# Kernel tuning notes

Measured on AMD Instinct MI355X. Metric: run time of the kernel, lower is better.

The kernel has to match this reference:

```python
import jax, jax.numpy as jnp
import numpy as np

K = 16          # NUM_PARTS (foreground parts); K+1 prototypes incl. background
D = 768         # EMBED_DIM
C = 200         # NUM_CLASSES
LN_EPS = 1e-6


def setup_inputs() -> dict:
    key = jax.random.key(0)
    k1, k2, k3, k4 = jax.random.split(key, 4)
    B, H, W = 32, 24, 24
    patch_features = jax.random.normal(k1, (B, H, W, D), dtype=jnp.float32)
    prototypes = 0.02 * jax.random.normal(k2, (K + 1, D), dtype=jnp.float32)
    ln_gamma = jnp.ones((D,), dtype=jnp.float32)
    ln_beta = jnp.zeros((D,), dtype=jnp.float32)
    # keras Dense default: glorot_uniform kernel, zero bias
    lim = np.sqrt(6.0 / (D + C)).astype(np.float32)
    w_cls = jax.random.uniform(k3, (D, C), dtype=jnp.float32, minval=-lim, maxval=lim)
    b_cls = jnp.zeros((C,), dtype=jnp.float32)
    return {
        "patch_features": patch_features,
        "prototypes": prototypes,
        "ln_gamma": ln_gamma,
        "ln_beta": ln_beta,
        "w_cls": w_cls,
        "b_cls": b_cls,
    }


def reference(patch_features, prototypes, ln_gamma, ln_beta, w_cls, b_cls):
    B, H, W, Dm = patch_features.shape
    P = H * W
    x = patch_features.reshape(B, P, Dm)                      # (B,P,D)

    # squared euclidean distance to K+1 prototypes, expressed as a GEMM:
    # ||z - p||^2 = ||z||^2 - 2 z.p + ||p||^2   -> (B,P,K+1)
    x_sq = jnp.sum(x * x, axis=-1, keepdims=True)             # (B,P,1)
    p_sq = jnp.sum(prototypes * prototypes, axis=-1)          # (K+1,)
    xp = jnp.einsum("bpd,kd->bpk", x, prototypes)             # (B,P,K+1)
    dists = x_sq - 2.0 * xp + p_sq                            # (B,P,K+1)

    # eval path: plain softmax over -distances
    a = jax.nn.softmax(-dists, axis=-1)                       # (B,P,K+1)

    # attention maps (B, K+1, H, W)
    A = jnp.transpose(a, (0, 2, 1)).reshape(B, K + 1, H, W)

    # weighted aggregation of patch features per part, normalized by P
    v_all = jnp.einsum("bpk,bpd->bkd", a, x) / jnp.float32(P) # (B,K+1,D)
    v_fg = v_all[:, :K, :]                                    # (B,K,D)

    # layernorm over last axis (eps=1e-6, learnable gamma/beta)
    mu = jnp.mean(v_fg, axis=-1, keepdims=True)
    var = jnp.mean(jnp.square(v_fg - mu), axis=-1, keepdims=True)
    v_norm = (v_fg - mu) * jax.lax.rsqrt(var + LN_EPS) * ln_gamma + ln_beta

    # shared per-part classifier + mean aggregation over parts
    logits_parts = jnp.einsum("bkd,dc->bkc", v_norm, w_cls) + b_cls  # (B,K,C)
    logits_agg = jnp.mean(logits_parts, axis=1)                      # (B,C)

    return (A, v_norm, logits_parts, logits_agg)
```

## Files before the change

### kernel.cpp

```cpp
#include <hip/hip_runtime.h>
#include <hip/hip_bf16.h>

#define B    32
#define P    576
#define D    768
#define K1   17
#define KFG  16
#define C    200
#define LN_EPS 1e-6f

typedef __attribute__((ext_vector_type(8))) short short8;
typedef __attribute__((ext_vector_type(4))) float f32x4;

__device__ inline unsigned short f2b(float f) {
    union { float f; unsigned u; } x; x.f = f;
    unsigned r = x.u + 0x7FFF + ((x.u >> 16) & 1);
    return (unsigned short)(r >> 16);
}

__global__ __launch_bounds__(256) void k_pre(const float* __restrict__ proto,
                                             float* __restrict__ psq,
                                             unsigned short* __restrict__ pbf) {
    const int k = blockIdx.x, t = threadIdx.x;
    float a0 = proto[k * D + t], a1 = proto[k * D + t + 256], a2 = proto[k * D + t + 512];
    pbf[k * D + t]       = f2b(a0);
    pbf[k * D + t + 256] = f2b(a1);
    pbf[k * D + t + 512] = f2b(a2);
    float s = a0 * a0 + a1 * a1 + a2 * a2;
    #pragma unroll
    for (int o = 1; o < 64; o <<= 1) s += __shfl_xor(s, o, 64);
    __shared__ float r[4];
    if ((t & 63) == 0) r[t >> 6] = s;
    __syncthreads();
    if (t == 0) psq[k] = r[0] + r[1] + r[2] + r[3];
}

__global__ __launch_bounds__(256, 4) void k_dots(const float* __restrict__ x,
                                                 const unsigned short* __restrict__ pbf,
                                                 const float* __restrict__ psq,
                                                 float* __restrict__ A_out,
                                                 float* __restrict__ apool) {
    __shared__ float scL[4][64][8];
    const int tile = blockIdx.x, b = blockIdx.y;
    const int t = threadIdx.x, wv = t >> 6, lane = t & 63;
    const int n = lane & 15, kq = lane >> 4;
    const int p0 = tile * 16;

    const float*          arow = x   + ((size_t)(b * P + p0 + n)) * D + wv * 192 + kq * 8;
    const unsigned short* brow = pbf + (size_t)n  * D + wv * 192 + kq * 8;
    const unsigned short* brw6 = pbf + (size_t)16 * D + wv * 192 + kq * 8;

    f32x4 acc0 = {0.f, 0.f, 0.f, 0.f};
    f32x4 acc1 = {0.f, 0.f, 0.f, 0.f};

    #pragma unroll
    for (int it = 0; it < 6; ++it) {
        const float* ap = arow + it * 32;
        float4 v0 = *(const float4*)(ap);
        float4 v1 = *(const float4*)(ap + 4);
        short8 A;
        A[0] = (short)f2b(v0.x); A[1] = (short)f2b(v0.y);
        A[2] = (short)f2b(v0.z); A[3] = (short)f2b(v0.w);
        A[4] = (short)f2b(v1.x); A[5] = (short)f2b(v1.y);
        A[6] = (short)f2b(v1.z); A[7] = (short)f2b(v1.w);
        short8 Bv = *(const short8*)(brow + it * 32);
        short8 B6 = *(const short8*)(brw6 + it * 32);
        acc0 = __builtin_amdgcn_mfma_f32_16x16x32_bf16(A, Bv, acc0, 0, 0, 0);
        acc1 = __builtin_amdgcn_mfma_f32_16x16x32_bf16(A, B6, acc1, 0, 0, 0);
    }

    #pragma unroll
    for (int r = 0; r < 4; ++r) {
        scL[wv][lane][r]     = acc0[r];
        scL[wv][lane][r + 4] = acc1[r];
    }
    __syncthreads();
    if (wv != 0) return;

    float s0[4], s1[4];
    #pragma unroll
    for (int r = 0; r < 4; ++r) {
        s0[r] = scL[0][lane][r]   + scL[1][lane][r]   + scL[2][lane][r]   + scL[3][lane][r];
        s1[r] = scL[0][lane][r+4] + scL[1][lane][r+4] + scL[2][lane][r+4] + scL[3][lane][r+4];
    }

    const float pq   = psq[n];
    const float pq16 = psq[16];
    float a_[4], a16[4], ap_[4];
    #pragma unroll
    for (int r = 0; r < 4; ++r) {
        float l0  = 2.f * s0[r] - pq;
        float l16 = 2.f * s1[r] - pq16;
        float mx = l0;
        #pragma unroll
        for (int o = 1; o < 16; o <<= 1) mx = fmaxf(mx, __shfl_xor(mx, o, 64));
        mx = fmaxf(mx, l16);
        float e0  = __expf(l0 - mx);
        float e16 = __expf(l16 - mx);
        float sum = e0;
        #pragma unroll
        for (int o = 1; o < 16; o <<= 1) sum += __shfl_xor(sum, o, 64);
        sum += e16;
        const float inv = 1.f / sum;
        a_[r]  = e0 * inv;
        a16[r] = e16 * inv;
        ap_[r] = a_[r] * (1.f / (float)P);
    }

    *(float4*)(A_out + ((size_t)b * K1 + n) * P + p0 + kq * 4) =
        make_float4(a_[0], a_[1], a_[2], a_[3]);
    if (n == 0)
        *(float4*)(A_out + ((size_t)b * K1 + 16) * P + p0 + kq * 4) =
            make_float4(a16[0], a16[1], a16[2], a16[3]);
    #pragma unroll
    for (int r = 0; r < 4; ++r)
        apool[((size_t)b * P + p0 + kq * 4 + r) * KFG + n] = ap_[r];
}

__global__ __launch_bounds__(256, 4) void k_pool(const float* __restrict__ x,
                                                 const float* __restrict__ apool,
                                                 float* __restrict__ vpart) {
    __shared__ float as_[192 * 16];
    const int dc = blockIdx.x, psl = blockIdx.y, b = blockIdx.z;
    const int t = threadIdx.x;

    const float* asrc = apool + ((size_t)b * P + psl * 192) * KFG;
    for (int i = t; i < 192 * 16; i += 256) as_[i] = asrc[i];
    __syncthreads();

    const int d = dc * 256 + t;
    const float* xp = x + ((size_t)b * P + psl * 192) * D + d;

    float acc[KFG];
    #pragma unroll
    for (int k = 0; k < KFG; ++k) acc[k] = 0.f;

    #pragma unroll 2
    for (int p = 0; p < 192; ++p) {
        float xv = xp[(size_t)p * D];
        float4 A0 = *(const float4*)(as_ + p * 16);
        float4 A1 = *(const float4*)(as_ + p * 16 + 4);
        float4 A2 = *(const float4*)(as_ + p * 16 + 8);
        float4 A3 = *(const float4*)(as_ + p * 16 + 12);
        acc[0]  += A0.x * xv; acc[1]  += A0.y * xv; acc[2]  += A0.z * xv; acc[3]  += A0.w * xv;
        acc[4]  += A1.x * xv; acc[5]  += A1.y * xv; acc[6]  += A1.z * xv; acc[7]  += A1.w * xv;
        acc[8]  += A2.x * xv; acc[9]  += A2.y * xv; acc[10] += A2.z * xv; acc[11] += A2.w * xv;
        acc[12] += A3.x * xv; acc[13] += A3.y * xv; acc[14] += A3.z * xv; acc[15] += A3.w * xv;
    }
    float* o = vpart + ((size_t)(psl * B + b) * KFG) * D + d;
    #pragma unroll
    for (int k = 0; k < KFG; ++k) o[(size_t)k * D] = acc[k];
}

__global__ __launch_bounds__(256) void k_ln(const float* __restrict__ vpart,
                                            const float* __restrict__ gamma,
                                            const float* __restrict__ beta,
                                            float* __restrict__ vnorm_out) {
    const int k = blockIdx.x, b = blockIdx.y, t = threadIdx.x;
    const int lane = t & 63, wv = t >> 6;

    float v[3]; float s1 = 0.f, s2 = 0.f;
    #pragma unroll
    for (int j = 0; j < 3; ++j) {
        const int d = t + j * 256;
        float s = vpart[((size_t)(0 * B + b) * KFG + k) * D + d]
                + vpart[((size_t)(1 * B + b) * KFG + k) * D + d]
                + vpart[((size_t)(2 * B + b) * KFG + k) * D + d];
        v[j] = s; s1 += s; s2 += s * s;
    }
    #pragma unroll
    for (int o = 1; o < 64; o <<= 1) {
        s1 += __shfl_xor(s1, o, 64);
        s2 += __shfl_xor(s2, o, 64);
    }
    __shared__ float r1[4], r2[4];
    if (lane == 0) { r1[wv] = s1; r2[wv] = s2; }
    __syncthreads();
    s1 = r1[0] + r1[1] + r1[2] + r1[3];
    s2 = r2[0] + r2[1] + r2[2] + r2[3];

    const float mean = s1 * (1.f / (float)D);
    const float var  = s2 * (1.f / (float)D) - mean * mean;
    const float rs   = rsqrtf(var + LN_EPS);

    #pragma unroll
    for (int j = 0; j < 3; ++j) {
        const int d = t + j * 256;
        float vn = (v[j] - mean) * rs * gamma[d] + beta[d];
        vnorm_out[((size_t)b * KFG + k) * D + d] = vn;
    }
}

__global__ __launch_bounds__(256) void k_cls(const float* __restrict__ vnorm,
                                             const float* __restrict__ W,
                                             float* __restrict__ lpart) {
    __shared__ float vs_[96 * 16];
    const int dq = blockIdx.x, b = blockIdx.y;
    const int c = threadIdx.x;

    for (int i = c; i < 96 * 16; i += 256) {
        int k = i / 96, dd = i - k * 96;
        vs_[dd * 16 + k] = vnorm[((size_t)b * KFG + k) * D + dq * 96 + dd];
    }
    __syncthreads();

    const int cc = c < C ? c : (C - 1);
    const float* Wp = W + (size_t)dq * 96 * C + cc;

    float acc[KFG];
    #pragma unroll
    for (int k = 0; k < KFG; ++k) acc[k] = 0.f;

    #pragma unroll 2
    for (int i = 0; i < 96; ++i) {
        float wl = Wp[(size_t)i * C];
        float4 V0 = *(const float4*)(vs_ + i * 16);
        float4 V1 = *(const float4*)(vs_ + i * 16 + 4);
        float4 V2 = *(const float4*)(vs_ + i * 16 + 8);
        float4 V3 = *(const float4*)(vs_ + i * 16 + 12);
        acc[0]  += V0.x * wl; acc[1]  += V0.y * wl; acc[2]  += V0.z * wl; acc[3]  += V0.w * wl;
        acc[4]  += V1.x * wl; acc[5]  += V1.y * wl; acc[6]  += V1.z * wl; acc[7]  += V1.w * wl;
        acc[8]  += V2.x * wl; acc[9]  += V2.y * wl; acc[10] += V2.z * wl; acc[11] += V2.w * wl;
        acc[12] += V3.x * wl; acc[13] += V3.y * wl; acc[14] += V3.z * wl; acc[15] += V3.w * wl;
    }
    if (c < C) {
        float* o = lpart + ((size_t)(dq * B + b) * KFG) * C + c;
        #pragma unroll
        for (int k = 0; k < KFG; ++k) o[(size_t)k * C] = acc[k];
    }
}

__global__ __launch_bounds__(256) void k_comb(const float* __restrict__ lpart,
                                              const float* __restrict__ bcls,
                                              float* __restrict__ parts,
                                              float* __restrict__ agg) {
    const int b = blockIdx.x, c = threadIdx.x;
    if (c >= C) return;
    const float bc = bcls[c];
    float s_agg = 0.f;
    #pragma unroll
    for (int k = 0; k < KFG; ++k) {
        float s = bc;
        #pragma unroll
        for (int dq = 0; dq < 8; ++dq)
            s += lpart[((size_t)(dq * B + b) * KFG + k) * C + c];
        parts[((size_t)b * KFG + k) * C + c] = s;
        s_agg += s;
    }
    agg[(size_t)b * C + c] = s_agg * (1.f / (float)KFG);
}

extern "C" void kernel_launch(void* const* d_in, const int* in_sizes, int n_in,
                              void* d_out, int out_size, void* d_ws, size_t ws_size,
                              hipStream_t stream) {
    const float* x     = (const float*)d_in[0];
    const float* proto = (const float*)d_in[1];
    const float* gamma = (const float*)d_in[2];
    const float* beta  = (const float*)d_in[3];
    const float* W     = (const float*)d_in[4];
    const float* bcls  = (const float*)d_in[5];

    float* out = (float*)d_out;
    float* A_out     = out;
    float* vnorm_out = out + 313344;
    float* parts_out = out + 706560;
    float* agg_out   = out + 808960;

    float* ws = (float*)d_ws;
    float* psq  = ws;
    unsigned short* pbf = (unsigned short*)(ws + 32);
    float* apool = ws + 32 + 6528;
    float* vpart = apool + 294912;
    float* lpart = vpart + 1179648;

    hipLaunchKernelGGL(k_pre,  dim3(K1),        dim3(256), 0, stream, proto, psq, pbf);
    hipLaunchKernelGGL(k_dots, dim3(36, B),     dim3(256), 0, stream, x, pbf, psq, A_out, apool);
    hipLaunchKernelGGL(k_pool, dim3(3, 3, B),   dim3(256), 0, stream, x, apool, vpart);
    hipLaunchKernelGGL(k_ln,   dim3(KFG, B),    dim3(256), 0, stream, vpart, gamma, beta, vnorm_out);
    hipLaunchKernelGGL(k_cls,  dim3(8, B),      dim3(256), 0, stream, vnorm_out, W, lpart);
    hipLaunchKernelGGL(k_comb, dim3(B),         dim3(256), 0, stream, lpart, bcls, parts_out, agg_out);
}
```

Before: 166.2 us.

## Restructure dots to single-wave blocks, split pool finer, drop LDS staging

k_dots now runs one wavefront per 16-patch tile covering the full D loop, which removes the LDS cross-wave reduction and barrier but leaves fewer threads per tile. k_pool splits patches into six slices of 96 instead of three of 192 and reads attention weights directly from global memory instead of staging them in LDS. k_ln also writes a transposed copy of the normalized vectors so k_cls can read them directly without an LDS transpose, and bf16 conversion uses packed intrinsics. The exchange is more global or L1 traffic, a larger vpart workspace, and an extra write in k_ln.

```diff
diff --git a/kernel.cpp b/kernel.cpp
--- a/kernel.cpp
+++ b/kernel.cpp
@@ -16,6 +16,16 @@
     union { float f; unsigned u; } x; x.f = f;
     unsigned r = x.u + 0x7FFF + ((x.u >> 16) & 1);
     return (unsigned short)(r >> 16);
+}
+
+__device__ inline short8 cvt8(float4 a, float4 b) {
+    union { unsigned u[4]; short8 s; } r;
+    union { __hip_bfloat162 h; unsigned u; } c;
+    c.h = __float22bfloat162_rn(make_float2(a.x, a.y)); r.u[0] = c.u;
+    c.h = __float22bfloat162_rn(make_float2(a.z, a.w)); r.u[1] = c.u;
+    c.h = __float22bfloat162_rn(make_float2(b.x, b.y)); r.u[2] = c.u;
+    c.h = __float22bfloat162_rn(make_float2(b.z, b.w)); r.u[3] = c.u;
+    return r.s;
 }
 
 __global__ __launch_bounds__(256) void k_pre(const float* __restrict__ proto,
@@ -35,62 +45,41 @@
     if (t == 0) psq[k] = r[0] + r[1] + r[2] + r[3];
 }
 
-__global__ __launch_bounds__(256, 4) void k_dots(const float* __restrict__ x,
-                                                 const unsigned short* __restrict__ pbf,
-                                                 const float* __restrict__ psq,
-                                                 float* __restrict__ A_out,
-                                                 float* __restrict__ apool) {
-    __shared__ float scL[4][64][8];
+__global__ __launch_bounds__(64, 2) void k_dots(const float* __restrict__ x,
+                                                const unsigned short* __restrict__ pbf,
+                                                const float* __restrict__ psq,
+                                                float* __restrict__ A_out,
+                                                float* __restrict__ apool) {
     const int tile = blockIdx.x, b = blockIdx.y;
-    const int t = threadIdx.x, wv = t >> 6, lane = t & 63;
+    const int lane = threadIdx.x;
     const int n = lane & 15, kq = lane >> 4;
     const int p0 = tile * 16;
 
-    const float*          arow = x   + ((size_t)(b * P + p0 + n)) * D + wv * 192 + kq * 8;
-    const unsigned short* brow = pbf + (size_t)n  * D + wv * 192 + kq * 8;
-    const unsigned short* brw6 = pbf + (size_t)16 * D + wv * 192 + kq * 8;
+    const float*          arow = x   + ((size_t)(b * P + p0 + n)) * D + kq * 8;
+    const unsigned short* brow = pbf + (size_t)n  * D + kq * 8;
+    const unsigned short* brw6 = pbf + (size_t)16 * D + kq * 8;
 
     f32x4 acc0 = {0.f, 0.f, 0.f, 0.f};
     f32x4 acc1 = {0.f, 0.f, 0.f, 0.f};
 
-    #pragma unroll
-    for (int it = 0; it < 6; ++it) {
-        const float* ap = arow + it * 32;
+    #pragma unroll 8
+    for (int s = 0; s < 24; ++s) {
+        const float* ap = arow + s * 32;
         float4 v0 = *(const float4*)(ap);
         float4 v1 = *(const float4*)(ap + 4);
-        short8 A;
-        A[0] = (short)f2b(v0.x); A[1] = (short)f2b(v0.y);
-        A[2] = (short)f2b(v0.z); A[3] = (short)f2b(v0.w);
-        A[4] = (short)f2b(v1.x); A[5] = (short)f2b(v1.y);
-        A[6] = (short)f2b(v1.z); A[7] = (short)f2b(v1.w);
-        short8 Bv = *(const short8*)(brow + it * 32);
-        short8 B6 = *(const short8*)(brw6 + it * 32);
+        short8 A  = cvt8(v0, v1);
+        short8 Bv = *(const short8*)(brow + s * 32);
+        short8 B6 = *(const short8*)(brw6 + s * 32);
         acc0 = __builtin_amdgcn_mfma_f32_16x16x32_bf16(A, Bv, acc0, 0, 0, 0);
         acc1 = __builtin_amdgcn_mfma_f32_16x16x32_bf16(A, B6, acc1, 0, 0, 0);
     }
 
+    const float pq = psq[n], pq16 = psq[16];
+    float a_[4], a16[4];
     #pragma unroll
     for (int r = 0; r < 4; ++r) {
-        scL[wv][lane][r]     = acc0[r];
-        scL[wv][lane][r + 4] = acc1[r];
-    }
-    __syncthreads();
-    if (wv != 0) return;
-
-    float s0[4], s1[4];
-    #pragma unroll
-    for (int r = 0; r < 4; ++r) {
-        s0[r] = scL[0][lane][r]   + scL[1][lane][r]   + scL[2][lane][r]   + scL[3][lane][r];
-        s1[r] = scL[0][lane][r+4] + scL[1][lane][r+4] + scL[2][lane][r+4] + scL[3][lane][r+4];
-    }
-
-    const float pq   = psq[n];
-    const float pq16 = psq[16];
-    float a_[4], a16[4], ap_[4];
-    #pragma unroll
-    for (int r = 0; r < 4; ++r) {
-        float l0  = 2.f * s0[r] - pq;
-        float l16 = 2.f * s1[r] - pq16;
+        float l0  = 2.f * acc0[r] - pq;
+        float l16 = 2.f * acc1[r] - pq16;
         float mx = l0;
         #pragma unroll
         for (int o = 1; o < 16; o <<= 1) mx = fmaxf(mx, __shfl_xor(mx, o, 64));
@@ -104,7 +93,6 @@
         const float inv = 1.f / sum;
         a_[r]  = e0 * inv;
         a16[r] = e16 * inv;
-        ap_[r] = a_[r] * (1.f / (float)P);
     }
 
     *(float4*)(A_out + ((size_t)b * K1 + n) * P + p0 + kq * 4) =
@@ -112,40 +100,38 @@
     if (n == 0)
         *(float4*)(A_out + ((size_t)b * K1 + 16) * P + p0 + kq * 4) =
             make_float4(a16[0], a16[1], a16[2], a16[3]);
+
+    const float invP = 1.f / (float)P;
     #pragma unroll
     for (int r = 0; r < 4; ++r)
-        apool[((size_t)b * P + p0 + kq * 4 + r) * KFG + n] = ap_[r];
+        apool[((size_t)b * P + p0 + kq * 4 + r) * KFG + n] = a_[r] * invP;
 }
 
 __global__ __launch_bounds__(256, 4) void k_pool(const float* __restrict__ x,
                                                  const float* __restrict__ apool,
                                                  float* __restrict__ vpart) {
-    __shared__ float as_[192 * 16];
     const int dc = blockIdx.x, psl = blockIdx.y, b = blockIdx.z;
     const int t = threadIdx.x;
-
-    const float* asrc = apool + ((size_t)b * P + psl * 192) * KFG;
-    for (int i = t; i < 192 * 16; i += 256) as_[i] = asrc[i];
-    __syncthreads();
-
     const int d = dc * 256 + t;
-    const float* xp = x + ((size_t)b * P + psl * 192) * D + d;
+
+    const float* aw = apool + ((size_t)b * P + psl * 96) * KFG;
+    const float* xp = x + ((size_t)b * P + psl * 96) * D + d;
 
     float acc[KFG];
     #pragma unroll
     for (int k = 0; k < KFG; ++k) acc[k] = 0.f;
 
-    #pragma unroll 2
-    for (int p = 0; p < 192; ++p) {
+    #pragma unroll 4
+    for (int p = 0; p < 96; ++p) {
         float xv = xp[(size_t)p * D];
-        float4 A0 = *(const float4*)(as_ + p * 16);
-        float4 A1 = *(const float4*)(as_ + p * 16 + 4);
-        float4 A2 = *(const float4*)(as_ + p * 16 + 8);
-        float4 A3 = *(const float4*)(as_ + p * 16 + 12);
-        acc[0]  += A0.x * xv; acc[1]  += A0.y * xv; acc[2]  += A0.z * xv; acc[3]  += A0.w * xv;
-        acc[4]  += A1.x * xv; acc[5]  += A1.y * xv; acc[6]  += A1.z * xv; acc[7]  += A1.w * xv;
-        acc[8]  += A2.x * xv; acc[9]  += A2.y * xv; acc[10] += A2.z * xv; acc[11] += A2.w * xv;
-        acc[12] += A3.x * xv; acc[13] += A3.y * xv; acc[14] += A3.z * xv; acc[15] += A3.w * xv;
+        f32x4 A0 = *(const f32x4*)(aw + p * 16);
+        f32x4 A1 = *(const f32x4*)(aw + p * 16 + 4);
+        f32x4 A2 = *(const f32x4*)(aw + p * 16 + 8);
+        f32x4 A3 = *(const f32x4*)(aw + p * 16 + 12);
+        acc[0]  += A0[0] * xv; acc[1]  += A0[1] * xv; acc[2]  += A0[2] * xv; acc[3]  += A0[3] * xv;
+        acc[4]  += A1[0] * xv; acc[5]  += A1[1] * xv; acc[6]  += A1[2] * xv; acc[7]  += A1[3] * xv;
+        acc[8]  += A2[0] * xv; acc[9]  += A2[1] * xv; acc[10] += A2[2] * xv; acc[11] += A2[3] * xv;
+        acc[12] += A3[0] * xv; acc[13] += A3[1] * xv; acc[14] += A3[2] * xv; acc[15] += A3[3] * xv;
     }
     float* o = vpart + ((size_t)(psl * B + b) * KFG) * D + d;
     #pragma unroll
@@ -155,7 +141,8 @@
 __global__ __launch_bounds__(256) void k_ln(const float* __restrict__ vpart,
                                             const float* __restrict__ gamma,
                                             const float* __restrict__ beta,
-                                            float* __restrict__ vnorm_out) {
+                                            float* __restrict__ vnorm_out,
+                                            float* __restrict__ vT) {
     const int k = blockIdx.x, b = blockIdx.y, t = threadIdx.x;
     const int lane = t & 63, wv = t >> 6;
 
@@ -163,9 +150,10 @@
     #pragma unroll
     for (int j = 0; j < 3; ++j) {
         const int d = t + j * 256;
-        float s = vpart[((size_t)(0 * B + b) * KFG + k) * D + d]
-                + vpart[((size_t)(1 * B + b) * KFG + k) * D + d]
-                + vpart[((size_t)(2 * B + b) * KFG + k) * D + d];
+        float s = 0.f;
+        #pragma unroll
+        for (int psl = 0; psl < 6; ++psl)
+            s += vpart[((size_t)(psl * B + b) * KFG + k) * D + d];
         v[j] = s; s1 += s; s2 += s * s;
     }
     #pragma unroll
@@ -188,40 +176,35 @@
         const int d = t + j * 256;
         float vn = (v[j] - mean) * rs * gamma[d] + beta[d];
         vnorm_out[((size_t)b * KFG + k) * D + d] = vn;
-    }
-}
-
-__global__ __launch_bounds__(256) void k_cls(const float* __restrict__ vnorm,
+        vT[((size_t)b * D + d) * KFG + k] = vn;
+    }
+}
+
+__global__ __launch_bounds__(256) void k_cls(const float* __restrict__ vT,
                                              const float* __restrict__ W,
                                              float* __restrict__ lpart) {
-    __shared__ float vs_[96 * 16];
     const int dq = blockIdx.x, b = blockIdx.y;
     const int c = threadIdx.x;
-
-    for (int i = c; i < 96 * 16; i += 256) {
-        int k = i / 96, dd = i - k * 96;
-        vs_[dd * 16 + k] = vnorm[((size_t)b * KFG + k) * D + dq * 96 + dd];
-    }
-    __syncthreads();
-
     const int cc = c < C ? c : (C - 1);
+
+    const float* vt = vT + ((size_t)b * D + dq * 96) * KFG;
     const float* Wp = W + (size_t)dq * 96 * C + cc;
 
     float acc[KFG];
     #pragma unroll
     for (int k = 0; k < KFG; ++k) acc[k] = 0.f;
 
-    #pragma unroll 2
+    #pragma unroll 4
     for (int i = 0; i < 96; ++i) {
         float wl = Wp[(size_t)i * C];
-        float4 V0 = *(const float4*)(vs_ + i * 16);
-        float4 V1 = *(const float4*)(vs_ + i * 16 + 4);
-        float4 V2 = *(const float4*)(vs_ + i * 16 + 8);
-        float4 V3 = *(const float4*)(vs_ + i * 16 + 12);
-        acc[0]  += V0.x * wl; acc[1]  += V0.y * wl; acc[2]  += V0.z * wl; acc[3]  += V0.w * wl;
-        acc[4]  += V1.x * wl; acc[5]  += V1.y * wl; acc[6]  += V1.z * wl; acc[7]  += V1.w * wl;
-        acc[8]  += V2.x * wl; acc[9]  += V2.y * wl; acc[10] += V2.z * wl; acc[11] += V2.w * wl;
-        acc[12] += V3.x * wl; acc[13] += V3.y * wl; acc[14] += V3.z * wl; acc[15] += V3.w * wl;
+        f32x4 V0 = *(const f32x4*)(vt + i * 16);
+        f32x4 V1 = *(const f32x4*)(vt + i * 16 + 4);
+        f32x4 V2 = *(const f32x4*)(vt + i * 16 + 8);
+        f32x4 V3 = *(const f32x4*)(vt + i * 16 + 12);
+        acc[0]  += V0[0] * wl; acc[1]  += V0[1] * wl; acc[2]  += V0[2] * wl; acc[3]  += V0[3] * wl;
+        acc[4]  += V1[0] * wl; acc[5]  += V1[1] * wl; acc[6]  += V1[2] * wl; acc[7]  += V1[3] * wl;
+        acc[8]  += V2[0] * wl; acc[9]  += V2[1] * wl; acc[10] += V2[2] * wl; acc[11] += V2[3] * wl;
+        acc[12] += V3[0] * wl; acc[13] += V3[1] * wl; acc[14] += V3[2] * wl; acc[15] += V3[3] * wl;
     }
     if (c < C) {
         float* o = lpart + ((size_t)(dq * B + b) * KFG) * C + c;
@@ -271,12 +254,13 @@
     unsigned short* pbf = (unsigned short*)(ws + 32);
     float* apool = ws + 32 + 6528;
     float* vpart = apool + 294912;
-    float* lpart = vpart + 1179648;
+    float* vT    = vpart + 2359296;
+    float* lpart = vT + 393216;
 
     hipLaunchKernelGGL(k_pre,  dim3(K1),        dim3(256), 0, stream, proto, psq, pbf);
-    hipLaunchKernelGGL(k_dots, dim3(36, B),     dim3(256), 0, stream, x, pbf, psq, A_out, apool);
-    hipLaunchKernelGGL(k_pool, dim3(3, 3, B),   dim3(256), 0, stream, x, apool, vpart);
-    hipLaunchKernelGGL(k_ln,   dim3(KFG, B),    dim3(256), 0, stream, vpart, gamma, beta, vnorm_out);
-    hipLaunchKernelGGL(k_cls,  dim3(8, B),      dim3(256), 0, stream, vnorm_out, W, lpart);
+    hipLaunchKernelGGL(k_dots, dim3(36, B),     dim3(64),  0, stream, x, pbf, psq, A_out, apool);
+    hipLaunchKernelGGL(k_pool, dim3(3, 6, B),   dim3(256), 0, stream, x, apool, vpart);
+    hipLaunchKernelGGL(k_ln,   dim3(KFG, B),    dim3(256), 0, stream, vpart, gamma, beta, vnorm_out, vT);
+    hipLaunchKernelGGL(k_cls,  dim3(8, B),      dim3(256), 0, stream, vT, W, lpart);
     hipLaunchKernelGGL(k_comb, dim3(B),         dim3(256), 0, stream, lpart, bcls, parts_out, agg_out);
 }
```

Result: faster. 147.8 us (-11.0%).
